# Kernel tuning notes

Measured on AMD Instinct MI355X. Metric: run time of the kernel, lower is better.

The kernel has to match this reference:

```python
import jax, jax.numpy as jnp
import numpy as np
import math

B, T, D, H, FFN_DIM, SE_HID = 16, 1024, 512, 8, 2048, 256
EPS = 1e-5  # torch LayerNorm default


def layer_norm(x, g, b):
    mu = jnp.mean(x, axis=-1, keepdims=True)
    var = jnp.mean((x - mu) ** 2, axis=-1, keepdims=True)
    return (x - mu) * jax.lax.rsqrt(var + EPS) * g + b


def setup_inputs() -> dict:
    key = jax.random.key(0)
    ks = jax.random.split(key, 8)
    s = 0.02
    return {
        "x": jax.random.normal(ks[0], (B, T, D), dtype=jnp.float32),
        "wq": jax.random.normal(ks[1], (D, D), dtype=jnp.float32) * s,
        "wk": jax.random.normal(ks[2], (D, D), dtype=jnp.float32) * s,
        "wv": jax.random.normal(ks[3], (D, D), dtype=jnp.float32) * s,
        "ln1_g": jnp.ones((D,), jnp.float32),
        "ln1_b": jnp.zeros((D,), jnp.float32),
        "se_w1": jax.random.normal(ks[4], (T, SE_HID), dtype=jnp.float32) * s,
        "se_w2": jax.random.normal(ks[5], (SE_HID, T), dtype=jnp.float32) * s,
        "ffn_g": jnp.ones((D,), jnp.float32),
        "ffn_b": jnp.zeros((D,), jnp.float32),
        "w1": jax.random.normal(ks[6], (D, FFN_DIM), dtype=jnp.float32) * s,
        "b1": jnp.zeros((FFN_DIM,), jnp.float32),
        "w2": jax.random.normal(ks[7], (FFN_DIM, D), dtype=jnp.float32) * s,
        "b2": jnp.zeros((D,), jnp.float32),
    }


def _forward(x, wq, wk, wv, ln1_g, ln1_b, se_w1, se_w2, ffn_g, ffn_b, w1, b1, w2, b2):
    # --- SE gate over the sequence axis: squeeze over feature dim D ---
    y = jnp.mean(x, axis=-1)                       # (B, T)
    gate = jax.nn.sigmoid(jax.nn.relu(y @ se_w1) @ se_w2)  # (B, T)
    x = x + x * gate[..., None]

    d = D // H
    n = layer_norm(x, ln1_g, ln1_b)
    q = (n @ wq).reshape(B, T, H, d)
    k = (n @ wk).reshape(B, T, H, d)
    v = (n @ wv).reshape(B, T, H, d)
    attn = jnp.einsum('bnhd,bmhd->bnmh', q, k) / math.sqrt(d)
    w = jax.nn.softmax(attn, axis=2)               # softmax over key dim m
    x = x + jnp.einsum('bnmh,bmhd->bnhd', w, v).reshape(B, T, D)

    # --- FFN (pre-norm, exact GELU as nn.GELU default) ---
    n2 = layer_norm(x, ffn_g, ffn_b)
    h = jax.nn.gelu(n2 @ w1 + b1, approximate=False)
    return x + (h @ w2 + b2)


def reference(x, wq, wk, wv, ln1_g, ln1_b, se_w1, se_w2, ffn_g, ffn_b, w1, b1, w2, b2):
    return _forward(x, wq, wk, wv, ln1_g, ln1_b, se_w1, se_w2, ffn_g, ffn_b, w1, b1, w2, b2)
```

## Files before the change

### kernel.cpp

```cpp
#include <hip/hip_runtime.h>

typedef unsigned int uint32;

using bf16x8 = __attribute__((ext_vector_type(8))) short;
using f32x4  = __attribute__((ext_vector_type(4))) float;

#define B_  16
#define T_  1024
#define D_  512
#define H_  8
#define HD_ 64
#define FFN_ 2048
#define SEH_ 256
#define EPS_ 1e-5f

#define AS1 __attribute__((address_space(1)))
#define AS3 __attribute__((address_space(3)))

__device__ __forceinline__ ushort f2bf(float f) {
  uint32 x = __float_as_uint(f);
  return (ushort)((x + 0x7fffu + ((x >> 16) & 1u)) >> 16);
}
__device__ __forceinline__ float bf2f(ushort u) {
  return __uint_as_float(((uint32)u) << 16);
}
__device__ __forceinline__ uint32 cvtpk(float a, float b) {
  uint32 r;
  asm("v_cvt_pk_bf16_f32 %0, %1, %2" : "=v"(r) : "v"(a), "v"(b));
  return r;
}
__device__ __forceinline__ float gelu_fast(float v) {
  float u = v * (0.7978845608f + 0.0356774081f * v * v);
  float e = __expf(2.0f * u);
  float t = 1.0f - 2.0f * __builtin_amdgcn_rcpf(e + 1.0f);
  return 0.5f * v * (1.0f + t);
}

__global__ __launch_bounds__(256) void cast_transpose_all_k(
    const float* __restrict__ wq, const float* __restrict__ wk,
    const float* __restrict__ wv, const float* __restrict__ w1,
    const float* __restrict__ w2, ushort* __restrict__ wqkvT,
    ushort* __restrict__ w1T, ushort* __restrict__ w2T) {
  __shared__ float tile[32][33];
  int bid = blockIdx.x;
  const float* W; ushort* WT; int K, N, bk, bn;
  if (bid < 768) {
    int w = bid >> 8, r = bid & 255;
    W = (w == 0) ? wq : (w == 1) ? wk : wv;
    WT = wqkvT + (size_t)w * 512 * 512;
    K = 512; N = 512; bk = (r >> 4) * 32; bn = (r & 15) * 32;
  } else if (bid < 1792) {
    int r = bid - 768;
    W = w1; WT = w1T; K = 512; N = 2048; bk = (r >> 6) * 32; bn = (r & 63) * 32;
  } else {
    int r = bid - 1792;
    W = w2; WT = w2T; K = 2048; N = 512; bk = (r >> 4) * 32; bn = (r & 15) * 32;
  }
  int lx = threadIdx.x & 31;
  int ly = threadIdx.x >> 5;
  #pragma unroll
  for (int i = ly; i < 32; i += 8)
    tile[i][lx] = W[(size_t)(bk + i) * N + bn + lx];
  __syncthreads();
  #pragma unroll
  for (int i = ly; i < 32; i += 8)
    WT[(size_t)(bn + i) * K + bk + lx] = f2bf(tile[lx][i]);
}

__global__ __launch_bounds__(256) void se_rowmean_k(const float* __restrict__ x,
                                                    float* __restrict__ y) {
  int row  = blockIdx.x * 4 + (threadIdx.x >> 6);
  int lane = threadIdx.x & 63;
  const float4* p = (const float4*)(x + (size_t)row * D_);
  float4 a = p[lane * 2];
  float4 b = p[lane * 2 + 1];
  float s = a.x + a.y + a.z + a.w + b.x + b.y + b.z + b.w;
  #pragma unroll
  for (int m = 1; m < 64; m <<= 1) s += __shfl_xor(s, m);
  if (lane == 0) y[row] = s * (1.0f / D_);
}

__global__ __launch_bounds__(256) void se_mlp1_k(const float* __restrict__ y,
                                                 const float* __restrict__ w1,
                                                 float* __restrict__ z) {
  __shared__ float yb[T_];
  __shared__ float part[8][32];
  int b = blockIdx.x, jt = blockIdx.y;
  int tid = threadIdx.x;
  #pragma unroll
  for (int i = 0; i < 4; i++) yb[tid + i * 256] = y[(size_t)b * T_ + tid + i * 256];
  __syncthreads();
  int tj = tid & 31, tk = tid >> 5;
  int j = jt * 32 + tj;
  const float* wp = w1 + (size_t)(tk * 128) * SEH_ + j;
  const float* yp = yb + tk * 128;
  float a0 = 0.f, a1 = 0.f, a2 = 0.f, a3 = 0.f;
  #pragma unroll
  for (int t = 0; t < 128; t += 4) {
    a0 += yp[t]     * wp[(t)     * SEH_];
    a1 += yp[t + 1] * wp[(t + 1) * SEH_];
    a2 += yp[t + 2] * wp[(t + 2) * SEH_];
    a3 += yp[t + 3] * wp[(t + 3) * SEH_];
  }
  part[tk][tj] = (a0 + a1) + (a2 + a3);
  __syncthreads();
  if (tid < 32) {
    float s = 0.f;
    #pragma unroll
    for (int k = 0; k < 8; k++) s += part[k][tid];
    z[(size_t)b * SEH_ + jt * 32 + tid] = fmaxf(s, 0.f);
  }
}

__global__ __launch_bounds__(256) void se_mlp2_k(const float* __restrict__ z,
                                                 const float* __restrict__ w2,
                                                 float* __restrict__ gate) {
  __shared__ float zb[SEH_];
  __shared__ float part[2][128];
  int b = blockIdx.x, bt = blockIdx.y;
  int tid = threadIdx.x;
  zb[tid & 255] = z[(size_t)b * SEH_ + (tid & 255)];
  __syncthreads();
  int tt = tid & 127, tk = tid >> 7;
  int t = bt * 128 + tt;
  const float* wp = w2 + (size_t)(tk * 128) * T_ + t;
  const float* zp = zb + tk * 128;
  float a0 = 0.f, a1 = 0.f, a2 = 0.f, a3 = 0.f;
  #pragma unroll
  for (int j = 0; j < 128; j += 4) {
    a0 += zp[j]     * wp[(j)     * T_];
    a1 += zp[j + 1] * wp[(j + 1) * T_];
    a2 += zp[j + 2] * wp[(j + 2) * T_];
    a3 += zp[j + 3] * wp[(j + 3) * T_];
  }
  part[tk][tt] = (a0 + a1) + (a2 + a3);
  __syncthreads();
  if (tid < 128) {
    float s = part[0][tid] + part[1][tid];
    gate[(size_t)b * T_ + bt * 128 + tid] = 1.0f / (1.0f + __expf(-s));
  }
}

__global__ __launch_bounds__(256) void gate_ln1_k(
    const float* __restrict__ x, const float* __restrict__ gate,
    const float* __restrict__ g, const float* __restrict__ beta,
    float* __restrict__ x1, ushort* __restrict__ nbuf) {
  int rid  = blockIdx.x * 4 + (threadIdx.x >> 6);
  int lane = threadIdx.x & 63;
  const float4* xr = (const float4*)(x + (size_t)rid * D_);
  float4 a = xr[lane * 2];
  float4 b = xr[lane * 2 + 1];
  float gv = 1.0f + gate[rid];
  a.x *= gv; a.y *= gv; a.z *= gv; a.w *= gv;
  b.x *= gv; b.y *= gv; b.z *= gv; b.w *= gv;
  float4* x1r = (float4*)(x1 + (size_t)rid * D_);
  x1r[lane * 2]     = a;
  x1r[lane * 2 + 1] = b;
  float s  = a.x + a.y + a.z + a.w + b.x + b.y + b.z + b.w;
  float ss = a.x*a.x + a.y*a.y + a.z*a.z + a.w*a.w + b.x*b.x + b.y*b.y + b.z*b.z + b.w*b.w;
  #pragma unroll
  for (int m = 1; m < 64; m <<= 1) { s += __shfl_xor(s, m); ss += __shfl_xor(ss, m); }
  float mu   = s * (1.0f / D_);
  float var  = ss * (1.0f / D_) - mu * mu;
  float rstd = rsqrtf(var + EPS_);
  const float4* gp = (const float4*)g;
  const float4* bp = (const float4*)beta;
  float4 g0 = gp[lane * 2], g1 = gp[lane * 2 + 1];
  float4 b0 = bp[lane * 2], b1 = bp[lane * 2 + 1];
  union { uint4 v; ushort u[8]; } pk;
  pk.u[0] = f2bf((a.x - mu) * rstd * g0.x + b0.x);
  pk.u[1] = f2bf((a.y - mu) * rstd * g0.y + b0.y);
  pk.u[2] = f2bf((a.z - mu) * rstd * g0.z + b0.z);
  pk.u[3] = f2bf((a.w - mu) * rstd * g0.w + b0.w);
  pk.u[4] = f2bf((b.x - mu) * rstd * g1.x + b1.x);
  pk.u[5] = f2bf((b.y - mu) * rstd * g1.y + b1.y);
  pk.u[6] = f2bf((b.z - mu) * rstd * g1.z + b1.z);
  pk.u[7] = f2bf((b.w - mu) * rstd * g1.w + b1.w);
  *(uint4*)(nbuf + (size_t)rid * D_ + lane * 8) = pk.v;
}

__global__ __launch_bounds__(256) void ln2_k(
    const float* __restrict__ x2, const float* __restrict__ g,
    const float* __restrict__ beta, ushort* __restrict__ nbuf) {
  int rid  = blockIdx.x * 4 + (threadIdx.x >> 6);
  int lane = threadIdx.x & 63;
  const float4* xr = (const float4*)(x2 + (size_t)rid * D_);
  float4 a = xr[lane * 2];
  float4 b = xr[lane * 2 + 1];
  float s  = a.x + a.y + a.z + a.w + b.x + b.y + b.z + b.w;
  float ss = a.x*a.x + a.y*a.y + a.z*a.z + a.w*a.w + b.x*b.x + b.y*b.y + b.z*b.z + b.w*b.w;
  #pragma unroll
  for (int m = 1; m < 64; m <<= 1) { s += __shfl_xor(s, m); ss += __shfl_xor(ss, m); }
  float mu   = s * (1.0f / D_);
  float var  = ss * (1.0f / D_) - mu * mu;
  float rstd = rsqrtf(var + EPS_);
  const float4* gp = (const float4*)g;
  const float4* bp = (const float4*)beta;
  float4 g0 = gp[lane * 2], g1 = gp[lane * 2 + 1];
  float4 b0 = bp[lane * 2], b1 = bp[lane * 2 + 1];
  union { uint4 v; ushort u[8]; } pk;
  pk.u[0] = f2bf((a.x - mu) * rstd * g0.x + b0.x);
  pk.u[1] = f2bf((a.y - mu) * rstd * g0.y + b0.y);
  pk.u[2] = f2bf((a.z - mu) * rstd * g0.z + b0.z);
  pk.u[3] = f2bf((a.w - mu) * rstd * g0.w + b0.w);
  pk.u[4] = f2bf((b.x - mu) * rstd * g1.x + b1.x);
  pk.u[5] = f2bf((b.y - mu) * rstd * g1.y + b1.y);
  pk.u[6] = f2bf((b.z - mu) * rstd * g1.z + b1.z);
  pk.u[7] = f2bf((b.w - mu) * rstd * g1.w + b1.w);
  *(uint4*)(nbuf + (size_t)rid * D_ + lane * 8) = pk.v;
}

#define MFMA16 __builtin_amdgcn_mfma_f32_16x16x32_bf16
template <int BN>
__global__ __launch_bounds__(512, 2) void gemm256_k(
    const ushort* __restrict__ A, const ushort* __restrict__ BT,
    int M, int N, int K,
    const float* __restrict__ bias, const float* __restrict__ resid,
    ushort* __restrict__ outB, ushort* __restrict__ outB2,
    ushort* __restrict__ vTout, float* __restrict__ outF, int epi) {
  constexpr int WNS   = BN / 4;
  constexpr int NT    = BN / 64;
  constexpr int NH    = NT / 2;
  constexpr int BROWS = BN / 8;
  constexpr int BJ    = BN / 64;
  __shared__ ushort smem[2 * 256 * 64 + 2 * BN * 64];
  ushort* As = smem;
  ushort* Bs = smem + 2 * 256 * 64;

  int tid  = threadIdx.x;
  int wave = tid >> 6;
  int lane = tid & 63;
  int quad = lane >> 4;
  int l15  = lane & 15;
  int wm   = wave >> 2;
  int wn   = wave & 3;
  int lr   = lane >> 3;
  int lcs  = (lane & 7) ^ lr;

  int nbk = N / BN;
  int bid = blockIdx.x;
  int xcd = bid & 7;
  int sb  = bid >> 3;
  int n0  = (sb % nbk) * BN;
  int m0  = ((sb / nbk) * 8 + xcd) * 256;

  f32x4 acc[8][NT];
  #pragma unroll
  for (int i = 0; i < 8; i++)
    #pragma unroll
    for (int j = 0; j < NT; j++) acc[i][j] = (f32x4){0.f, 0.f, 0.f, 0.f};

  const ushort* Ag = A  + (size_t)(m0 + wave * 32 + lr) * K + lcs * 8;
  const ushort* Bg = BT + (size_t)(n0 + wave * BROWS + lr) * K + lcs * 8;

  auto STAGE = [&](int t, int buf) {
    int ko = t * 64;
    ushort* da = As + buf * (256 * 64) + wave * (32 * 64);
    #pragma unroll
    for (int j = 0; j < 4; j++)
      __builtin_amdgcn_global_load_lds((const AS1 void*)(Ag + ko + (size_t)(j * 8) * K),
                                       (AS3 void*)(da + j * 512), 16, 0, 0);
    ushort* db = Bs + buf * (BN * 64) + wave * (BROWS * 64);
    #pragma unroll
    for (int j = 0; j < BJ; j++)
      __builtin_amdgcn_global_load_lds((const AS1 void*)(Bg + ko + (size_t)(j * 8) * K),
                                       (AS3 void*)(db + j * 512), 16, 0, 0);
  };

  int ntt = K >> 6;
  STAGE(0, 0);
  STAGE(1, 1);
  if constexpr (BN == 256) asm volatile("s_waitcnt vmcnt(8)" ::: "memory");
  else                     asm volatile("s_waitcnt vmcnt(6)" ::: "memory");
  __builtin_amdgcn_s_barrier();

  const ushort* Arow = As + (wm * 128 + l15) * 64;
  const ushort* Brow = Bs + (wn * WNS + l15) * 64;
  int c0 = ((0 + quad) ^ (l15 & 7)) * 8;
  int c1 = ((4 + quad) ^ (l15 & 7)) * 8;

  for (int t = 0; t < ntt; ++t) {
    const ushort* Ab = Arow + (t & 1) * (256 * 64);
    const ushort* Bb = Brow + (t & 1) * (BN * 64);
    bf16x8 a[4][2], b[NT][2];

    #pragma unroll
    for (int m4 = 0; m4 < 4; m4++) {
      a[m4][0] = *(const bf16x8*)(Ab + m4 * 1024 + c0);
      a[m4][1] = *(const bf16x8*)(Ab + m4 * 1024 + c1);
    }
    #pragma unroll
    for (int h = 0; h < NH; h++) {
      b[h][0] = *(const bf16x8*)(Bb + h * 1024 + c0);
      b[h][1] = *(const bf16x8*)(Bb + h * 1024 + c1);
    }
    __builtin_amdgcn_s_barrier();
    asm volatile("s_waitcnt lgkmcnt(0)" ::: "memory");
    __builtin_amdgcn_sched_barrier(0);
    __builtin_amdgcn_s_setprio(1);
    #pragma unroll
    for (int m4 = 0; m4 < 4; m4++)
      #pragma unroll
      for (int h = 0; h < NH; h++) {
        acc[m4][h] = MFMA16(a[m4][0], b[h][0], acc[m4][h], 0, 0, 0);
        acc[m4][h] = MFMA16(a[m4][1], b[h][1], acc[m4][h], 0, 0, 0);
      }
    __builtin_amdgcn_s_setprio(0);
    __builtin_amdgcn_s_barrier();

    #pragma unroll
    for (int h = 0; h < NH; h++) {
      b[NH + h][0] = *(const bf16x8*)(Bb + (NH + h) * 1024 + c0);
      b[NH + h][1] = *(const bf16x8*)(Bb + (NH + h) * 1024 + c1);
    }
    __builtin_amdgcn_s_barrier();
    asm volatile("s_waitcnt lgkmcnt(0)" ::: "memory");
    __builtin_amdgcn_sched_barrier(0);
    __builtin_amdgcn_s_setprio(1);
    #pragma unroll
    for (int m4 = 0; m4 < 4; m4++)
      #pragma unroll
      for (int h = 0; h < NH; h++) {
        acc[m4][NH + h] = MFMA16(a[m4][0], b[NH + h][0], acc[m4][NH + h], 0, 0, 0);
        acc[m4][NH + h] = MFMA16(a[m4][1], b[NH + h][1], acc[m4][NH + h], 0, 0, 0);
      }
    __builtin_amdgcn_s_setprio(0);
    __builtin_amdgcn_s_barrier();

    #pragma unroll
    for (int m4 = 0; m4 < 4; m4++) {
      a[m4][0] = *(const bf16x8*)(Ab + (4 + m4) * 1024 + c0);
      a[m4][1] = *(const bf16x8*)(Ab + (4 + m4) * 1024 + c1);
    }
    __builtin_amdgcn_s_barrier();
    asm volatile("s_waitcnt lgkmcnt(0)" ::: "memory");
    __builtin_amdgcn_sched_barrier(0);
    __builtin_amdgcn_s_setprio(1);
    #pragma unroll
    for (int m4 = 0; m4 < 4; m4++)
      #pragma unroll
      for (int h = 0; h < NH; h++) {
        acc[4 + m4][h] = MFMA16(a[m4][0], b[h][0], acc[4 + m4][h], 0, 0, 0);
        acc[4 + m4][h] = MFMA16(a[m4][1], b[h][1], acc[4 + m4][h], 0, 0, 0);
      }
    __builtin_amdgcn_s_setprio(0);
    __builtin_amdgcn_s_barrier();

    __builtin_amdgcn_s_setprio(1);
    #pragma unroll
    for (int m4 = 0; m4 < 4; m4++)
      #pragma unroll
      for (int h = 0; h < NH; h++) {
        acc[4 + m4][NH + h] = MFMA16(a[m4][0], b[NH + h][0], acc[4 + m4][NH + h], 0, 0, 0);
        acc[4 + m4][NH + h] = MFMA16(a[m4][1], b[NH + h][1], acc[4 + m4][NH + h], 0, 0, 0);
      }
    __builtin_amdgcn_s_setprio(0);

    if (t + 1 < ntt) {
      if (t + 2 < ntt) {
        STAGE(t + 2, t & 1);
        if constexpr (BN == 256) asm volatile("s_waitcnt vmcnt(8)" ::: "memory");
        else                     asm volatile("s_waitcnt vmcnt(6)" ::: "memory");
      } else {
        asm volatile("s_waitcnt vmcnt(0)" ::: "memory");
      }
      __builtin_amdgcn_s_barrier();
    }
  }

  int colbase = n0 + wn * WNS;
  if (epi == 2) {
    #pragma unroll
    for (int nt = 0; nt < NT; nt++) {
      int n = colbase + nt * 16 + l15;
      float bv = bias[n];
      #pragma unroll
      for (int mt = 0; mt < 8; mt++) {
        int m = m0 + wm * 128 + mt * 16 + quad * 4;
        #pragma unroll
        for (int r = 0; r < 4; r++) {
          size_t idx = (size_t)(m + r) * N + n;
          outF[idx] = acc[mt][nt][r] + bv + resid[idx];
        }
      }
    }
  } else {
    __syncthreads();
    if (epi == 3 && n0 >= 1024) {
      constexpr int TST = 136;
      ushort* tb = smem + wave * (32 * TST);
      #pragma unroll
      for (int nt = 0; nt < NT; nt++) {
        int dloc = nt * 16 + l15;
        #pragma unroll
        for (int mt = 0; mt < 8; mt++) {
          ushort4 pk;
          pk.x = f2bf(acc[mt][nt][0]);
          pk.y = f2bf(acc[mt][nt][1]);
          pk.z = f2bf(acc[mt][nt][2]);
          pk.w = f2bf(acc[mt][nt][3]);
          *(ushort4*)(tb + dloc * TST + mt * 16 + quad * 4) = pk;
        }
      }
      int dbase = (n0 - 1024) + wn * WNS;
      int bb = m0 >> 10;
      int tg = (m0 & 1023) + wm * 128 + l15 * 8;
      #pragma unroll
      for (int j = 0; j < 8; j++) {
        int dloc = j * 4 + quad;
        int d = dbase + dloc;
        int hh = d >> 6, dd = d & 63;
        uint4 vv = *(const uint4*)(tb + dloc * TST + l15 * 8);
        *(uint4*)(vTout + (((size_t)bb * 8 + hh) * 64 + dd) * 1024 + tg) = vv;
      }
    } else {
      constexpr int RS  = WNS + 8;
      constexpr int LPR = WNS / 8;
      constexpr int RPS = 64 / LPR;
      ushort* tb = smem + wave * (32 * RS);
      ushort* gout; int ldN; float scl;
      if (epi == 1) { gout = outB; ldN = N; scl = 1.0f; }
      else {
        gout = (n0 < 512) ? outB : outB2; ldN = 512;
        scl = (n0 < 512) ? 0.18033688011112042f : 1.0f;
      }
      int ncol = (epi == 1) ? colbase : ((n0 & 511) + wn * WNS);
      float bv[NT];
      #pragma unroll
      for (int nt = 0; nt < NT; nt++)
        bv[nt] = (epi == 1) ? bias[colbase + nt * 16 + l15] : 0.0f;
      int rrow = lane / LPR;
      int seg  = lane % LPR;
      int mrow0 = m0 + wm * 128;
      #pragma unroll
      for (int mtg = 0; mtg < 4; mtg++) {
        #pragma unroll
        for (int mh = 0; mh < 2; mh++) {
          int mt = mtg * 2 + mh;
          #pragma unroll
          for (int nt = 0; nt < NT; nt++) {
            #pragma unroll
            for (int r = 0; r < 4; r++) {
              float v = (epi == 1) ? gelu_fast(acc[mt][nt][r] + bv[nt])
                                   : acc[mt][nt][r] * scl;
              tb[(mh * 16 + quad * 4 + r) * RS + nt * 16 + l15] = f2bf(v);
            }
          }
        }
        #pragma unroll
        for (int it = 0; it < 32 / RPS; it++) {
          int rl = it * RPS + rrow;
          uint4 v = *(const uint4*)(tb + rl * RS + seg * 8);
          *(uint4*)(gout + (size_t)(mrow0 + mtg * 32 + rl) * ldN + ncol + seg * 8) = v;
        }
      }
    }
  }
}

__global__ __launch_bounds__(512, 2) void attn_k(
    const ushort* __restrict__ q, const ushort* __restrict__ k,
    const ushort* __restrict__ vT, const float* __restrict__ x1,
    float* __restrict__ out) {
  __shared__ ushort Ks[2 * 64 * 64];
  __shared__ ushort Vs[2 * 64 * 64];
  __shared__ ushort Ps[256 * 64];
  int bid = blockIdx.x;
  int xcd = bid & 7;
  int j   = bid >> 3;
  int qt  = j & 3;
  int pair = xcd * 16 + (j >> 2);
  int b = pair >> 3;
  int h = pair & 7;
  int t0 = qt * 256;
  int tid  = threadIdx.x;
  int wave = tid >> 6;
  int lane = tid & 63;
  int quad = lane >> 4;
  int l15  = lane & 15;

  int row8 = lane >> 3;
  int csw  = ((lane & 7) ^ row8) * 8;
  const ushort* kst = k + ((size_t)(b * T_ + wave * 8 + row8)) * D_ + h * HD_ + csw;
  const ushort* vst = vT + ((size_t)((b * 8 + h) * 64 + wave * 8 + row8)) * 1024 + csw;
  ushort* KsW = Ks + wave * 512;
  ushort* VsW = Vs + wave * 512;

  auto STAGE = [&](int kt, int buf) {
    __builtin_amdgcn_global_load_lds((const AS1 void*)(kst + (size_t)kt * 64 * D_),
                                     (AS3 void*)(KsW + buf * 4096), 16, 0, 0);
    __builtin_amdgcn_global_load_lds((const AS1 void*)(vst + kt * 64),
                                     (AS3 void*)(VsW + buf * 4096), 16, 0, 0);
  };

  STAGE(0, 0);

  const ushort* qp0 = q + ((size_t)(b * T_ + t0 + wave * 16 + l15)) * D_ + h * HD_;
  const ushort* qp1 = qp0 + (size_t)128 * D_;
  bf16x8 aq0 = *(const bf16x8*)(qp0 + quad * 8);
  bf16x8 aq1 = *(const bf16x8*)(qp0 + 32 + quad * 8);
  bf16x8 aq2 = *(const bf16x8*)(qp1 + quad * 8);
  bf16x8 aq3 = *(const bf16x8*)(qp1 + 32 + quad * 8);

  int rsw0 = ((quad)     ^ (l15 & 7)) << 3;
  int rsw1 = ((quad + 4) ^ (l15 & 7)) << 3;

  float l_part[2][4] = {{0.f, 0.f, 0.f, 0.f}, {0.f, 0.f, 0.f, 0.f}};
  f32x4 o0[4], o1[4];
  #pragma unroll
  for (int dt = 0; dt < 4; dt++) {
    o0[dt] = (f32x4){0.f, 0.f, 0.f, 0.f};
    o1[dt] = (f32x4){0.f, 0.f, 0.f, 0.f};
  }

  asm volatile("s_waitcnt vmcnt(0)" ::: "memory");
  __syncthreads();

  for (int kt = 0; kt < 16; kt++) {
    int buf = kt & 1;
    if (kt + 1 < 16) STAGE(kt + 1, buf ^ 1);
    const ushort* Kb = Ks + buf * 4096;
    const ushort* Vb = Vs + buf * 4096;

    #pragma unroll
    for (int nt = 0; nt < 4; nt++) {
      const ushort* krow = Kb + (nt * 16 + l15) * 64;
      bf16x8 bk0 = *(const bf16x8*)(krow + rsw0);
      bf16x8 bk1 = *(const bf16x8*)(krow + rsw1);
      f32x4 z = (f32x4){0.f, 0.f, 0.f, 0.f};
      f32x4 s0 = MFMA16(aq0, bk0, z, 0, 0, 0);
      s0 = MFMA16(aq1, bk1, s0, 0, 0, 0);
      f32x4 s1 = MFMA16(aq2, bk0, z, 0, 0, 0);
      s1 = MFMA16(aq3, bk1, s1, 0, 0, 0);

      float p0[4], p1[4];
      #pragma unroll
      for (int r = 0; r < 4; r++) {
        p0[r] = __builtin_amdgcn_exp2f(s0[r]);
        p1[r] = __builtin_amdgcn_exp2f(s1[r]);
        l_part[0][r] += p0[r];
        l_part[1][r] += p1[r];
      }
      int cps = nt * 2 + (l15 >> 3);
      int cbase = l15 & 7;
      #pragma unroll
      for (int hs = 0; hs < 2; hs++) {
        uint32 u01 = cvtpk(hs ? p1[0] : p0[0], hs ? p1[1] : p0[1]);
        uint32 u23 = cvtpk(hs ? p1[2] : p0[2], hs ? p1[3] : p0[3]);
        int rb = hs * 128 + wave * 16 + quad * 4;
        #pragma unroll
        for (int r = 0; r < 4; r++) {
          int off = (rb + r) * 64 + ((cps ^ ((quad * 4 + r) & 7)) << 3) + cbase;
          uint32 uu = (r < 2) ? u01 : u23;
          Ps[off] = (ushort)((r & 1) ? (uu >> 16) : uu);
        }
      }
    }

    const ushort* prow = Ps + (wave * 16 + l15) * 64;
    bf16x8 ap0 = *(const bf16x8*)(prow + rsw0);
    bf16x8 ap1 = *(const bf16x8*)(prow + rsw1);
    bf16x8 ap2 = *(const bf16x8*)(prow + 8192 + rsw0);
    bf16x8 ap3 = *(const bf16x8*)(prow + 8192 + rsw1);
    #pragma unroll
    for (int dt = 0; dt < 4; dt++) {
      const ushort* vrow = Vb + (dt * 16 + l15) * 64;
      bf16x8 bv0 = *(const bf16x8*)(vrow + rsw0);
      bf16x8 bv1 = *(const bf16x8*)(vrow + rsw1);
      o0[dt] = MFMA16(ap0, bv0, o0[dt], 0, 0, 0);
      o0[dt] = MFMA16(ap1, bv1, o0[dt], 0, 0, 0);
      o1[dt] = MFMA16(ap2, bv0, o1[dt], 0, 0, 0);
      o1[dt] = MFMA16(ap3, bv1, o1[dt], 0, 0, 0);
    }

    __syncthreads();
  }

  #pragma unroll
  for (int s = 0; s < 2; s++) {
    f32x4* oo = s ? o1 : o0;
    #pragma unroll
    for (int r = 0; r < 4; r++) {
      float l = l_part[s][r];
      l += __shfl_xor(l, 1);
      l += __shfl_xor(l, 2);
      l += __shfl_xor(l, 4);
      l += __shfl_xor(l, 8);
      float inv = 1.0f / l;
      int qrow = t0 + s * 128 + wave * 16 + quad * 4 + r;
      size_t base = ((size_t)(b * T_ + qrow)) * D_ + h * HD_;
      #pragma unroll
      for (int dt = 0; dt < 4; dt++) {
        size_t idx = base + dt * 16 + l15;
        out[idx] = x1[idx] + oo[dt][r] * inv;
      }
    }
  }
}

extern "C" void kernel_launch(void* const* d_in, const int* in_sizes, int n_in,
                              void* d_out, int out_size, void* d_ws, size_t ws_size,
                              hipStream_t stream) {
  (void)in_sizes; (void)n_in; (void)out_size; (void)ws_size;
  const float* x     = (const float*)d_in[0];
  const float* wq    = (const float*)d_in[1];
  const float* wk    = (const float*)d_in[2];
  const float* wv    = (const float*)d_in[3];
  const float* ln1_g = (const float*)d_in[4];
  const float* ln1_b = (const float*)d_in[5];
  const float* se_w1 = (const float*)d_in[6];
  const float* se_w2 = (const float*)d_in[7];
  const float* ffn_g = (const float*)d_in[8];
  const float* ffn_b = (const float*)d_in[9];
  const float* w1    = (const float*)d_in[10];
  const float* b1    = (const float*)d_in[11];
  const float* w2    = (const float*)d_in[12];
  const float* b2    = (const float*)d_in[13];
  float* out = (float*)d_out;
  char* ws = (char*)d_ws;

  constexpr size_t X1_OFF   = 0;
  constexpr size_t N_OFF    = 33554432;
  constexpr size_t Q_OFF    = 50331648;
  constexpr size_t K_OFF    = 67108864;
  constexpr size_t V_OFF    = 83886080;
  constexpr size_t H_OFF    = 50331648;
  constexpr size_t WQKV_OFF = 117440512;
  constexpr size_t W1T_OFF  = 119013376;
  constexpr size_t W2T_OFF  = 121110528;
  constexpr size_t Y_OFF    = 123207680;
  constexpr size_t Z_OFF    = 123273216;
  constexpr size_t GATE_OFF = 123289600;

  float*  x1    = (float*)(ws + X1_OFF);
  ushort* nbuf  = (ushort*)(ws + N_OFF);
  ushort* qb    = (ushort*)(ws + Q_OFF);
  ushort* kb    = (ushort*)(ws + K_OFF);
  ushort* vT    = (ushort*)(ws + V_OFF);
  ushort* hb    = (ushort*)(ws + H_OFF);
  ushort* wqkvT = (ushort*)(ws + WQKV_OFF);
  ushort* w1T   = (ushort*)(ws + W1T_OFF);
  ushort* w2T   = (ushort*)(ws + W2T_OFF);
  float*  yv    = (float*)(ws + Y_OFF);
  float*  zv    = (float*)(ws + Z_OFF);
  float*  gate  = (float*)(ws + GATE_OFF);

  const int M = B_ * T_;

  cast_transpose_all_k<<<2816, 256, 0, stream>>>(wq, wk, wv, w1, w2, wqkvT, w1T, w2T);

  se_rowmean_k<<<M / 4, 256, 0, stream>>>(x, yv);
  se_mlp1_k<<<dim3(B_, 8), 256, 0, stream>>>(yv, se_w1, zv);
  se_mlp2_k<<<dim3(B_, 8), 256, 0, stream>>>(zv, se_w2, gate);

  gate_ln1_k<<<M / 4, 256, 0, stream>>>(x, gate, ln1_g, ln1_b, x1, nbuf);

  gemm256_k<128><<<(M / 256) * (1536 / 128), 512, 0, stream>>>(
      nbuf, wqkvT, M, 1536, D_, nullptr, nullptr, qb, kb, vT, nullptr, 3);

  attn_k<<<B_ * H_ * (T_ / 256), 512, 0, stream>>>(qb, kb, vT, x1, out);

  ln2_k<<<M / 4, 256, 0, stream>>>(out, ffn_g, ffn_b, nbuf);

  gemm256_k<256><<<(M / 256) * (FFN_ / 256), 512, 0, stream>>>(
      nbuf, w1T, M, FFN_, D_, b1, nullptr, hb, nullptr, nullptr, nullptr, 1);
  gemm256_k<128><<<(M / 256) * (D_ / 128), 512, 0, stream>>>(
      hb, w2T, M, D_, FFN_, b2, out, nullptr, nullptr, nullptr, out, 2);
}
```

Before: 331.7 us.

## Simplify GEMM main loop to single-stage prefetch with one barrier per tile

Replaces the hand-scheduled GEMM main loop with a simpler one. The old loop ran two tiles ahead and used split B/A fragment loads, many s_barriers, explicit vmcnt waits, and MFMA priority raising. The new loop prefetches only the next tile at the top of each iteration, loads all B fragments at once, and ends with a __syncthreads. This cuts barrier and waitcnt overhead and the register pressure from splitting fragments, but the prefetch now runs only one tile ahead. It also relies on __syncthreads for the async global_load_lds waits, which may serialize global latency with compute.

```diff
diff --git a/kernel.cpp b/kernel.cpp
--- a/kernel.cpp
+++ b/kernel.cpp
@@ -220,7 +220,6 @@
     ushort* __restrict__ vTout, float* __restrict__ outF, int epi) {
   constexpr int WNS   = BN / 4;
   constexpr int NT    = BN / 64;
-  constexpr int NH    = NT / 2;
   constexpr int BROWS = BN / 8;
   constexpr int BJ    = BN / 64;
   __shared__ ushort smem[2 * 256 * 64 + 2 * BN * 64];
@@ -269,10 +268,7 @@
 
   int ntt = K >> 6;
   STAGE(0, 0);
-  STAGE(1, 1);
-  if constexpr (BN == 256) asm volatile("s_waitcnt vmcnt(8)" ::: "memory");
-  else                     asm volatile("s_waitcnt vmcnt(6)" ::: "memory");
-  __builtin_amdgcn_s_barrier();
+  __syncthreads();
 
   const ushort* Arow = As + (wm * 128 + l15) * 64;
   const ushort* Brow = Bs + (wn * WNS + l15) * 64;
@@ -280,92 +276,43 @@
   int c1 = ((4 + quad) ^ (l15 & 7)) * 8;
 
   for (int t = 0; t < ntt; ++t) {
-    const ushort* Ab = Arow + (t & 1) * (256 * 64);
-    const ushort* Bb = Brow + (t & 1) * (BN * 64);
-    bf16x8 a[4][2], b[NT][2];
-
+    int cur = t & 1;
+    if (t + 1 < ntt) STAGE(t + 1, cur ^ 1);
+    const ushort* Ab = Arow + cur * (256 * 64);
+    const ushort* Bb = Brow + cur * (BN * 64);
+
+    bf16x8 b[NT][2], a[4][2];
+    #pragma unroll
+    for (int h = 0; h < NT; h++) {
+      b[h][0] = *(const bf16x8*)(Bb + h * 1024 + c0);
+      b[h][1] = *(const bf16x8*)(Bb + h * 1024 + c1);
+    }
     #pragma unroll
     for (int m4 = 0; m4 < 4; m4++) {
       a[m4][0] = *(const bf16x8*)(Ab + m4 * 1024 + c0);
       a[m4][1] = *(const bf16x8*)(Ab + m4 * 1024 + c1);
     }
     #pragma unroll
-    for (int h = 0; h < NH; h++) {
-      b[h][0] = *(const bf16x8*)(Bb + h * 1024 + c0);
-      b[h][1] = *(const bf16x8*)(Bb + h * 1024 + c1);
-    }
-    __builtin_amdgcn_s_barrier();
-    asm volatile("s_waitcnt lgkmcnt(0)" ::: "memory");
-    __builtin_amdgcn_sched_barrier(0);
-    __builtin_amdgcn_s_setprio(1);
-    #pragma unroll
     for (int m4 = 0; m4 < 4; m4++)
       #pragma unroll
-      for (int h = 0; h < NH; h++) {
+      for (int h = 0; h < NT; h++) {
         acc[m4][h] = MFMA16(a[m4][0], b[h][0], acc[m4][h], 0, 0, 0);
         acc[m4][h] = MFMA16(a[m4][1], b[h][1], acc[m4][h], 0, 0, 0);
       }
-    __builtin_amdgcn_s_setprio(0);
-    __builtin_amdgcn_s_barrier();
-
-    #pragma unroll
-    for (int h = 0; h < NH; h++) {
-      b[NH + h][0] = *(const bf16x8*)(Bb + (NH + h) * 1024 + c0);
-      b[NH + h][1] = *(const bf16x8*)(Bb + (NH + h) * 1024 + c1);
-    }
-    __builtin_amdgcn_s_barrier();
-    asm volatile("s_waitcnt lgkmcnt(0)" ::: "memory");
-    __builtin_amdgcn_sched_barrier(0);
-    __builtin_amdgcn_s_setprio(1);
-    #pragma unroll
-    for (int m4 = 0; m4 < 4; m4++)
-      #pragma unroll
-      for (int h = 0; h < NH; h++) {
-        acc[m4][NH + h] = MFMA16(a[m4][0], b[NH + h][0], acc[m4][NH + h], 0, 0, 0);
-        acc[m4][NH + h] = MFMA16(a[m4][1], b[NH + h][1], acc[m4][NH + h], 0, 0, 0);
-      }
-    __builtin_amdgcn_s_setprio(0);
-    __builtin_amdgcn_s_barrier();
-
     #pragma unroll
     for (int m4 = 0; m4 < 4; m4++) {
       a[m4][0] = *(const bf16x8*)(Ab + (4 + m4) * 1024 + c0);
       a[m4][1] = *(const bf16x8*)(Ab + (4 + m4) * 1024 + c1);
     }
-    __builtin_amdgcn_s_barrier();
-    asm volatile("s_waitcnt lgkmcnt(0)" ::: "memory");
-    __builtin_amdgcn_sched_barrier(0);
-    __builtin_amdgcn_s_setprio(1);
     #pragma unroll
     for (int m4 = 0; m4 < 4; m4++)
       #pragma unroll
-      for (int h = 0; h < NH; h++) {
+      for (int h = 0; h < NT; h++) {
         acc[4 + m4][h] = MFMA16(a[m4][0], b[h][0], acc[4 + m4][h], 0, 0, 0);
         acc[4 + m4][h] = MFMA16(a[m4][1], b[h][1], acc[4 + m4][h], 0, 0, 0);
       }
-    __builtin_amdgcn_s_setprio(0);
-    __builtin_amdgcn_s_barrier();
-
-    __builtin_amdgcn_s_setprio(1);
-    #pragma unroll
-    for (int m4 = 0; m4 < 4; m4++)
-      #pragma unroll
-      for (int h = 0; h < NH; h++) {
-        acc[4 + m4][NH + h] = MFMA16(a[m4][0], b[NH + h][0], acc[4 + m4][NH + h], 0, 0, 0);
-        acc[4 + m4][NH + h] = MFMA16(a[m4][1], b[NH + h][1], acc[4 + m4][NH + h], 0, 0, 0);
-      }
-    __builtin_amdgcn_s_setprio(0);
-
-    if (t + 1 < ntt) {
-      if (t + 2 < ntt) {
-        STAGE(t + 2, t & 1);
-        if constexpr (BN == 256) asm volatile("s_waitcnt vmcnt(8)" ::: "memory");
-        else                     asm volatile("s_waitcnt vmcnt(6)" ::: "memory");
-      } else {
-        asm volatile("s_waitcnt vmcnt(0)" ::: "memory");
-      }
-      __builtin_amdgcn_s_barrier();
-    }
+
+    __syncthreads();
   }
 
   int colbase = n0 + wn * WNS;
@@ -385,7 +332,6 @@
       }
     }
   } else {
-    __syncthreads();
     if (epi == 3 && n0 >= 1024) {
       constexpr int TST = 136;
       ushort* tb = smem + wave * (32 * TST);
```

New measurement: 309.0 us. -6.9%, faster.
